# Performance work log

Hardware: AMD Instinct MI355X
Metric: run time of the kernel (lower is better)

The kernel has to match this reference:

```python
import jax, jax.numpy as jnp
import numpy as np

BS, NA, HW, C, HEADS = 16, 256, 1024, 512, 8
FEAT_RES = 32  # hw = feat_res**2


def setup_inputs() -> dict:
    key = jax.random.key(0)
    ks = jax.random.split(key, 16)

    def lin_w(k, din, dout):
        return (jax.random.normal(k, (din, dout), jnp.float32) / np.sqrt(din)).astype(jnp.float32)

    inp = {
        "tok_agent": jax.random.normal(ks[0], (BS, NA, C), jnp.float32),
        "enc_feat_supp": jax.random.normal(ks[1], (BS, HW, C), jnp.float32),
        "enc_feat_query": jax.random.normal(ks[2], (BS, HW, C), jnp.float32),
        # projection weights stored as [in, out]
        "W_qa": lin_w(ks[3], C, C), "b_qa": jnp.zeros((C,), jnp.float32),
        "W_ks": lin_w(ks[4], C, C), "b_ks": jnp.zeros((C,), jnp.float32),
        "W_ka": lin_w(ks[5], C, C), "b_ka": jnp.zeros((C,), jnp.float32),
        "W_vs": lin_w(ks[6], C, C), "b_vs": jnp.zeros((C,), jnp.float32),
        # FFN: c -> 3c -> c
        "W_f1": lin_w(ks[7], C, 3 * C), "b_f1": jnp.zeros((3 * C,), jnp.float32),
        "W_f2": lin_w(ks[8], 3 * C, C), "b_f2": jnp.zeros((C,), jnp.float32),
    }
    return inp


def reference(tok_agent, enc_feat_supp, enc_feat_query,
              W_qa, b_qa, W_ks, b_ks, W_ka, b_ka, W_vs, b_vs,
              W_f1, b_f1, W_f2, b_f2):
    bs, na, c = tok_agent.shape
    hw = enc_feat_supp.shape[1]
    feat_res = int(round(np.sqrt(hw)))
    d_k_sqrt = np.float32(np.sqrt(c // HEADS))

    qa = tok_agent @ W_qa + b_qa                 # [bs, na, c]
    ks_ = enc_feat_supp @ W_ks + b_ks            # [bs, hw, c]
    qq = enc_feat_query @ W_qa + b_qa            # NOTE: original reuses qa_linear
    ka = tok_agent @ W_ka + b_ka                 # [bs, na, c]
    vs = enc_feat_supp @ W_vs + b_vs             # [bs, hw, c]

    scores_as = jnp.einsum('bac,bhc->bah', qa, ks_) / d_k_sqrt   # [bs, na, hw]
    scores_qa = jnp.einsum('bhc,bac->bha', qq, ka) / d_k_sqrt    # [bs, hw, na]

    # align_mat[b,i,j] = (argmax_a scores_as[b,a,i] == argmax_a scores_qa[b,j,a])
    a_idx = jnp.argmax(scores_as, axis=1)        # [bs, hw]
    b_idx = jnp.argmax(scores_qa, axis=2)        # [bs, hw]
    align = jnp.where(a_idx[:, :, None] == b_idx[:, None, :],
                      jnp.float32(0.0), jnp.float32(-1e6))       # [bs, hw, hw]

    # scores_sa @ scores_aq: [bs,hw,na] @ [bs,na,hw]
    logits = jnp.einsum('bai,bja->bij', scores_as, scores_qa)    # [bs, hw, hw]
    scores_qs = jax.nn.softmax(logits + align, axis=-1)

    # scores_qs^T @ vs : out[b,j,c] = sum_i scores_qs[b,i,j] * vs[b,i,c]
    dec = jnp.einsum('bij,bic->bjc', scores_qs, vs)              # [bs, hw, c]
    dec = jax.nn.relu(dec @ W_f1 + b_f1) @ W_f2 + b_f2           # FFN (dropout = eval identity)

    # raw memory reinterpretation, as in torch .view
    return dec.reshape(bs, c, feat_res, -1)
```

## Files before the change

kernel.cpp:

```cpp
#include <hip/hip_runtime.h>

typedef float          f32x4  __attribute__((ext_vector_type(4)));
typedef short          bf16x8 __attribute__((ext_vector_type(8)));
typedef _Float16       f16x8  __attribute__((ext_vector_type(8)));
typedef unsigned short u16x4  __attribute__((ext_vector_type(4)));

static constexpr int kBS = 16;
static constexpr int kHW = 1024;

__device__ __forceinline__ unsigned short f2bf(float x) {
  union { float f; unsigned int u; } v; v.f = x;
  unsigned int r = v.u + 0x7fffu + ((v.u >> 16) & 1u);
  return (unsigned short)(r >> 16);
}
__device__ __forceinline__ float bf2f(unsigned short h) {
  union { unsigned int u; float f; } v; v.u = ((unsigned int)h) << 16;
  return v.f;
}
__device__ __forceinline__ unsigned short h2u(_Float16 h) {
  union { _Float16 h; unsigned short u; } v; v.h = h; return v.u;
}

__device__ __forceinline__ void split2h(float x, unsigned short& u0, unsigned short& u1) {
  _Float16 h0 = (_Float16)x;
  if (fabsf(x) < 6.1035156e-05f) h0 = (_Float16)0.f;
  const float r = (x - (float)h0) * 4096.f;
  u0 = h2u(h0);
  u1 = h2u((_Float16)r);
}

__global__ __launch_bounds__(256)
void split_act2h(const f32x4* __restrict__ X, u16x4* __restrict__ P0,
                 u16x4* __restrict__ P1, int n4)
{
  int i = blockIdx.x * 256 + threadIdx.x;
  if (i >= n4) return;
  f32x4 x = X[i];
  u16x4 s0, s1;
#pragma unroll
  for (int u = 0; u < 4; ++u) {
    unsigned short a, b;
    split2h(x[u], a, b);
    s0[u] = a; s1[u] = b;
  }
  P0[i] = s0; P1[i] = s1;
}

__global__ __launch_bounds__(256)
void split_wT2h(const float* __restrict__ Wm, unsigned short* __restrict__ T0,
                unsigned short* __restrict__ T1, int K, int N)
{
  __shared__ float ts[32][33];
  const int k0 = blockIdx.x * 32, n0 = blockIdx.y * 32;
  const int tx = threadIdx.x, ty = threadIdx.y;
#pragma unroll
  for (int r = 0; r < 4; ++r)
    ts[ty + r * 8][tx] = Wm[(size_t)(k0 + ty + r * 8) * N + n0 + tx];
  __syncthreads();
#pragma unroll
  for (int r = 0; r < 4; ++r) {
    const int n = ty + r * 8;
    const size_t off = (size_t)(n0 + n) * K + k0 + tx;
    unsigned short a, b;
    split2h(ts[tx][n], a, b);
    T0[off] = a; T1[off] = b;
  }
}

template<bool F16>
__global__ __launch_bounds__(256)
void split_wT1(const float* __restrict__ Wm, unsigned short* __restrict__ T0,
               int K, int N)
{
  __shared__ float ts[32][33];
  const int k0 = blockIdx.x * 32, n0 = blockIdx.y * 32;
  const int tx = threadIdx.x, ty = threadIdx.y;
#pragma unroll
  for (int r = 0; r < 4; ++r)
    ts[ty + r * 8][tx] = Wm[(size_t)(k0 + ty + r * 8) * N + n0 + tx];
  __syncthreads();
#pragma unroll
  for (int r = 0; r < 4; ++r) {
    const int n = ty + r * 8;
    const float x = ts[tx][n];
    const size_t off = (size_t)(n0 + n) * K + k0 + tx;
    T0[off] = F16 ? h2u((_Float16)x) : f2bf(x);
  }
}

__device__ __forceinline__ void stage_tile(const unsigned short* src, int K,
                                           unsigned short* ldst, int wv, int lane)
{
#pragma unroll
  for (int i = 0; i < 2; ++i) {
    const int s   = wv * 128 + i * 64 + lane;
    const int row = s >> 2;
    const int gc  = ((s & 3) ^ ((row >> 1) & 3)) * 8;
    __builtin_amdgcn_global_load_lds(
        (const __attribute__((address_space(1))) void*)(src + (size_t)row * K + gc),
        (__attribute__((address_space(3))) void*)(ldst + ((wv * 128 + i * 64) << 3)),
        16, 0, 0);
  }
}

template<int ORD, int KU, bool DBUF, int OUTM, bool BIAS, bool RELU, bool F16IN>
__global__ __launch_bounds__(256)
void gke(const unsigned short* __restrict__ A0, const unsigned short* __restrict__ A1,
         const unsigned short* __restrict__ B0, const unsigned short* __restrict__ B1,
         const float* __restrict__ bias,
         float* __restrict__ Cf, unsigned short* __restrict__ O0,
         unsigned short* __restrict__ O1,
         int K, int ldc, long sA, long sB, long sC, long sBias, float scale)
{
  constexpr int NP  = ORD + 1;
  constexpr int NT  = 2 * NP;
  constexpr int TPP = KU * NT;
  static_assert(!DBUF || TPP * 2 == 16, "vmcnt constant assumes 16 loads/phase");
  extern __shared__ __align__(16) unsigned short lds[];

  const int tid  = threadIdx.x;
  const int wv   = tid >> 6, lane = tid & 63;
  const int wr   = wv >> 1,  wc   = wv & 1;
  const int cr   = lane & 15, cg  = lane >> 4;
  const int bm   = blockIdx.x * 128, bn = blockIdx.y * 128;

  const size_t zA = (size_t)blockIdx.z * (size_t)sA;
  const size_t zB = (size_t)blockIdx.z * (size_t)sB;
  const size_t zC = (size_t)blockIdx.z * (size_t)sC;
  const size_t zBias = (size_t)blockIdx.z * (size_t)sBias;

  const unsigned short* srcs[NT];
  srcs[0] = A0 + zA + (size_t)bm * K;
  if (NP == 2) srcs[1] = A1 + zA + (size_t)bm * K;
  srcs[NP + 0] = B0 + zB + (size_t)bn * K;
  if (NP == 2) srcs[NP + 1] = B1 + zB + (size_t)bn * K;

  f32x4 acc0[4][4], acc1[4][4];
#pragma unroll
  for (int i = 0; i < 4; ++i)
#pragma unroll
    for (int j = 0; j < 4; ++j)
#pragma unroll
      for (int r = 0; r < 4; ++r) {
        acc0[i][j][r] = 0.f;
        if (ORD == 1) acc1[i][j][r] = 0.f;
      }

#define STAGE_PH(ph, buf)                                                       \
  {                                                                             \
    _Pragma("unroll")                                                           \
    for (int u = 0; u < KU; ++u)                                                \
      _Pragma("unroll")                                                         \
      for (int t = 0; t < NT; ++t)                                              \
        stage_tile(srcs[t] + ((ph) * KU + u) * 32, K,                           \
                   lds + (size_t)((buf) * TPP + u * NT + t) * 4096, wv, lane);  \
  }
#define LOADA(u, pa)                                                            \
  {                                                                             \
    _Pragma("unroll")                                                           \
    for (int f = 0; f < 4; ++f) {                                               \
      const int ra = wr * 64 + f * 16 + cr;                                     \
      af[f] = *(const bf16x8*)&lb[(size_t)((u) * NT + (pa)) * 4096 +            \
                                  (ra * 4 + (cg ^ ((ra >> 1) & 3))) * 8];       \
    }                                                                           \
  }
#define DOPB(u, pb, ACC)                                                        \
  {                                                                             \
    bf16x8 bfr[4];                                                              \
    _Pragma("unroll")                                                           \
    for (int f = 0; f < 4; ++f) {                                               \
      const int rb = wc * 64 + f * 16 + cr;                                     \
      bfr[f] = *(const bf16x8*)&lb[(size_t)((u) * NT + NP + (pb)) * 4096 +      \
                                   (rb * 4 + (cg ^ ((rb >> 1) & 3))) * 8];      \
    }                                                                           \
    _Pragma("unroll")                                                           \
    for (int i = 0; i < 4; ++i)                                                 \
      _Pragma("unroll")                                                         \
      for (int j = 0; j < 4; ++j) {                                             \
        if constexpr (F16IN)                                                    \
          ACC[i][j] = __builtin_amdgcn_mfma_f32_16x16x32_f16(                   \
              __builtin_bit_cast(f16x8, af[i]), __builtin_bit_cast(f16x8, bfr[j]), \
              ACC[i][j], 0, 0, 0);                                              \
        else                                                                    \
          ACC[i][j] = __builtin_amdgcn_mfma_f32_16x16x32_bf16(af[i], bfr[j],    \
              ACC[i][j], 0, 0, 0);                                              \
      }                                                                         \
  }
#define COMPUTE_PH(buf)                                                         \
  {                                                                             \
    const unsigned short* lb = lds + (size_t)(buf) * TPP * 4096;                \
    bf16x8 af[4];                                                               \
    _Pragma("unroll")                                                           \
    for (int u = 0; u < KU; ++u) {                                              \
      if constexpr (ORD == 1) {                                                 \
        LOADA(u, 0); DOPB(u, 0, acc0); DOPB(u, 1, acc1);                        \
        LOADA(u, 1); DOPB(u, 0, acc1);                                          \
      } else {                                                                  \
        LOADA(u, 0); DOPB(u, 0, acc0);                                          \
      }                                                                         \
    }                                                                           \
  }

  const int nph = K / (32 * KU);
  if constexpr (!DBUF) {
    for (int ph = 0; ph < nph; ++ph) {
      if (ph) __syncthreads();
      STAGE_PH(ph, 0);
      __syncthreads();
      COMPUTE_PH(0);
    }
  } else {
    STAGE_PH(0, 0);
    STAGE_PH(1, 1);
    for (int ph = 0; ph < nph; ++ph) {
      if (ph + 1 < nph) asm volatile("s_waitcnt vmcnt(16)" ::: "memory");
      else              asm volatile("s_waitcnt vmcnt(0)" ::: "memory");
      __builtin_amdgcn_sched_barrier(0);
      __builtin_amdgcn_s_barrier();
      COMPUTE_PH(ph & 1);
      __builtin_amdgcn_s_barrier();
      __builtin_amdgcn_sched_barrier(0);
      if (ph + 2 < nph) STAGE_PH(ph + 2, ph & 1);
    }
  }
#undef STAGE_PH
#undef LOADA
#undef DOPB
#undef COMPUTE_PH

  const float RS = 2.44140625e-4f;
  float* CfB = Cf + zC;
  unsigned short* O0B = O0 + zC;
  unsigned short* O1B = O1 + zC;
#pragma unroll
  for (int fm = 0; fm < 4; ++fm) {
#pragma unroll
    for (int fn = 0; fn < 4; ++fn) {
      const int n  = bn + wc * 64 + fn * 16 + cr;
      const int m0 = bm + wr * 64 + fm * 16 + 4 * cg;
      float bv = 0.f;
      if (BIAS) bv = bias[zBias + n];
      if (OUTM == 4) {
        u16x4 o;
#pragma unroll
        for (int r = 0; r < 4; ++r) {
          float x = acc0[fm][fn][r];
          if constexpr (ORD == 1) x += acc1[fm][fn][r] * RS;
          x = x * scale + bv;
          if (RELU) x = fmaxf(x, 0.f);
          o[r] = f2bf(x);
        }
        *(u16x4*)(O0B + (size_t)n * ldc + m0) = o;
      } else {
#pragma unroll
        for (int r = 0; r < 4; ++r) {
          float x = acc0[fm][fn][r];
          if constexpr (ORD == 1) x += acc1[fm][fn][r] * RS;
          x = x * scale + bv;
          if (RELU) x = fmaxf(x, 0.f);
          const size_t off = (size_t)(m0 + r) * ldc + n;
          if (OUTM == 0) CfB[off] = x;
          else if (OUTM == 3) O0B[off] = f2bf(x);
          else {
            unsigned short a, b;
            split2h(x, a, b);
            O0B[off] = a; O1B[off] = b;
            if (OUTM == 2) CfB[off] = x;
          }
        }
      }
    }
  }
}

__global__ __launch_bounds__(256)
void row_argmax4(const float* __restrict__ X, int* __restrict__ out)
{
  const int row = blockIdx.x * 4 + (threadIdx.x >> 6);
  const float* xr = X + (size_t)row * 256;
  const int lane = threadIdx.x & 63;
  float best = -3.0e38f;
  int bi = 0;
#pragma unroll
  for (int t = 0; t < 4; ++t) {
    const int a = lane + (t << 6);
    const float x = xr[a];
    if (x > best) { best = x; bi = a; }
  }
#pragma unroll
  for (int off = 32; off >= 1; off >>= 1) {
    const float ov = __shfl_xor(best, off);
    const int   oi = __shfl_xor(bi, off);
    if (ov > best || (ov == best && oi < bi)) { best = ov; bi = oi; }
  }
  if (lane == 0) out[row] = bi;
}

__global__ __launch_bounds__(256)
void softmax_T(const float* __restrict__ Lg, const int* __restrict__ aidx,
               const int* __restrict__ bidx, unsigned short* __restrict__ PT,
               int ihalf)
{
  __shared__ int bj[1024];
  __shared__ unsigned short tile[1024 * 17];
  const int tid = threadIdx.x;
  const int i0  = blockIdx.x * 16;
  const int b   = blockIdx.y;
  const int r   = tid >> 4;
  const int l16 = tid & 15;

  for (int j = tid; j < 1024; j += 256) bj[j] = bidx[(b << 10) + j];
  __syncthreads();

  const int ai  = aidx[(b << 10) + (ihalf << 9) + i0 + r];
  const float* Lr = Lg + ((size_t)b * 512 + i0 + r) * 1024;
  const int jb = l16 * 64;

  float x[64];
  float mx = -3.0e38f;
#pragma unroll
  for (int q = 0; q < 16; ++q) {
    f32x4 f = *(const f32x4*)(Lr + jb + (q << 2));
#pragma unroll
    for (int u = 0; u < 4; ++u) {
      const int j = jb + (q << 2) + u;
      float t = f[u];
      if (bj[j] != ai) t -= 1e6f;
      x[(q << 2) + u] = t;
      mx = fmaxf(mx, t);
    }
  }
#pragma unroll
  for (int off = 8; off >= 1; off >>= 1) mx = fmaxf(mx, __shfl_xor(mx, off));
  float s = 0.f;
#pragma unroll
  for (int k = 0; k < 64; ++k) { float e = expf(x[k] - mx); x[k] = e; s += e; }
#pragma unroll
  for (int off = 8; off >= 1; off >>= 1) s += __shfl_xor(s, off);
  const float inv = 1.f / s;

#pragma unroll
  for (int k = 0; k < 64; ++k)
    tile[(jb + k) * 17 + r] = f2bf(x[k] * inv);
  __syncthreads();

  for (int j = tid; j < 1024; j += 256) {
    const unsigned short* tp = &tile[j * 17];
    unsigned int w[8];
#pragma unroll
    for (int q = 0; q < 8; ++q)
      w[q] = (unsigned int)tp[2 * q] | ((unsigned int)tp[2 * q + 1] << 16);
    const size_t off = ((size_t)b << 20) + ((size_t)j << 10) + (ihalf << 9) + i0;
    unsigned int* dst = (unsigned int*)(PT + off);
    *(uint4*)dst       = make_uint4(w[0], w[1], w[2], w[3]);
    *((uint4*)dst + 1) = make_uint4(w[4], w[5], w[6], w[7]);
  }
}

extern "C" void kernel_launch(void* const* d_in, const int* in_sizes, int n_in,
                              void* d_out, int out_size, void* d_ws, size_t ws_size,
                              hipStream_t stream)
{
  (void)in_sizes; (void)n_in; (void)out_size; (void)ws_size;

  const float* tok  = (const float*)d_in[0];
  const float* supp = (const float*)d_in[1];
  const float* qry  = (const float*)d_in[2];
  const float* W_qa = (const float*)d_in[3];
  const float* b_qa = (const float*)d_in[4];
  const float* W_ks = (const float*)d_in[5];
  const float* b_ks = (const float*)d_in[6];
  const float* W_ka = (const float*)d_in[7];
  const float* b_ka = (const float*)d_in[8];
  const float* W_vs = (const float*)d_in[9];
  const float* b_vs = (const float*)d_in[10];
  const float* W_f1 = (const float*)d_in[11];
  const float* b_f1 = (const float*)d_in[12];
  const float* W_f2 = (const float*)d_in[13];
  const float* b_f2 = (const float*)d_in[14];

  auto kProj  = &gke<1,2,false,1,true ,false,true >;
  auto kScore = &gke<1,2,true ,2,false,false,true >;
  auto kLogit = &gke<1,2,false,0,false,false,true >;
  auto kVsT   = &gke<0,4,false,4,true ,false,true >;
  auto kPV    = &gke<0,4,false,3,false,false,false>;
  auto kFFN1  = &gke<0,4,false,3,true ,true ,false>;
  auto kFFN2  = &gke<0,4,false,0,true ,false,false>;
  hipFuncSetAttribute((const void*)kProj,  hipFuncAttributeMaxDynamicSharedMemorySize, 65536);
  hipFuncSetAttribute((const void*)kScore, hipFuncAttributeMaxDynamicSharedMemorySize, 131072);
  hipFuncSetAttribute((const void*)kLogit, hipFuncAttributeMaxDynamicSharedMemorySize, 65536);
  hipFuncSetAttribute((const void*)kVsT,   hipFuncAttributeMaxDynamicSharedMemorySize, 65536);
  hipFuncSetAttribute((const void*)kPV,    hipFuncAttributeMaxDynamicSharedMemorySize, 65536);
  hipFuncSetAttribute((const void*)kFFN1,  hipFuncAttributeMaxDynamicSharedMemorySize, 65536);
  hipFuncSetAttribute((const void*)kFFN2,  hipFuncAttributeMaxDynamicSharedMemorySize, 65536);

  char* W = (char*)d_ws;
  constexpr size_t MiB = 1048576;
  auto U = [&](double off) { return (unsigned short*)(W + (size_t)(off * MiB)); };
  auto F = [&](double off) { return (float*)(W + (size_t)(off * MiB)); };
  auto I = [&](double off) { return (int*)(W + (size_t)(off * MiB)); };

  const double oTOK0=0, oTOK1=4, oQTF=0, oSUP0=0, oSAF=0, oPT=0;
  const double oWQAT=16, oWKAT=17.5, oWKST=19, oWVST=20.5;
  const double oQA0=22, oQA1=26, oDEC=32, oKA0=34, oKA1=38;
  const double oQRY0=46, oQRY1=62, oQTP0=46, oQTP1=54;
  const double oSUP1=62, oVST=62, oSAP0=78, oSAP1=86;
  const double oQQ0=94, oQQ1=110, oLG=94, oMID=62;
  const double oWF1=142, oWF2=143.5, oBIA=148, oIDXB=150, oIDXA=150.0625;
  const double hP = 0.5;

  const dim3 B256(256), BW(32, 8);
  float* dummyF = F(oLG);
  unsigned short* dummyU = U(oLG);

  hipMemcpyAsync(W + (size_t)(oBIA * MiB), b_qa, 2048, hipMemcpyDeviceToDevice, stream);
  hipMemcpyAsync(W + (size_t)(oBIA * MiB) + 2048, b_ka, 2048, hipMemcpyDeviceToDevice, stream);

  split_wT2h<<<dim3(16,16), BW, 0, stream>>>(W_qa, U(oWQAT), U(oWQAT+hP), 512, 512);
  split_wT2h<<<dim3(16,16), BW, 0, stream>>>(W_ka, U(oWKAT), U(oWKAT+hP), 512, 512);
  split_wT2h<<<dim3(16,16), BW, 0, stream>>>(W_ks, U(oWKST), U(oWKST+hP), 512, 512);
  split_wT1<true><<<dim3(16,16), BW, 0, stream>>>(W_vs, U(oWVST), 512, 512);
  split_act2h<<<dim3(2048), B256, 0, stream>>>((const f32x4*)tok, (u16x4*)U(oTOK0), (u16x4*)U(oTOK1), 524288);
  kProj<<<dim3(32,4,2), B256, 65536, stream>>>(
      U(oTOK0),U(oTOK1), U(oWQAT),U(oWQAT+hP),
      F(oBIA), dummyF, U(oQA0),U(oQA1), 512, 512, 0, 786432, 6291456, 512, 1.f);
  split_act2h<<<dim3(8192), B256, 0, stream>>>((const f32x4*)qry, (u16x4*)U(oQRY0), (u16x4*)U(oQRY1), 2097152);
  kProj<<<dim3(128,4,1), B256, 65536, stream>>>(
      U(oQRY0),U(oQRY1), U(oWQAT),U(oWQAT+hP),
      b_qa, dummyF, U(oQQ0),U(oQQ1), 512, 512, 0,0,0,0, 1.f);
  kScore<<<dim3(8,2,16), B256, 131072, stream>>>(
      U(oQQ0),U(oQQ1), U(oKA0),U(oKA1),
      nullptr, F(oQTF), U(oQTP0),U(oQTP1), 512, 256,
      524288, 131072, 262144, 0, 0.125f);
  row_argmax4<<<dim3(kBS * kHW / 4), B256, 0, stream>>>(F(oQTF), I(oIDXB));
  split_act2h<<<dim3(8192), B256, 0, stream>>>((const f32x4*)supp, (u16x4*)U(oSUP0), (u16x4*)U(oSUP1), 2097152);
  kProj<<<dim3(128,4,1), B256, 65536, stream>>>(
      U(oSUP0),U(oSUP1), U(oWKST),U(oWKST+hP),
      b_ks, dummyF, U(oQQ0),U(oQQ1), 512, 512, 0,0,0,0, 1.f);
  kVsT<<<dim3(8,4,16), B256, 65536, stream>>>(
      U(oSUP0),dummyU, U(oWVST),dummyU,
      b_vs, dummyF, U(oVST),dummyU, 512, 1024,
      524288, 0, 524288, 0, 1.f);
  kScore<<<dim3(8,2,16), B256, 131072, stream>>>(
      U(oQQ0),U(oQQ1), U(oQA0),U(oQA1),
      nullptr, F(oSAF), U(oSAP0),U(oSAP1), 512, 256,
      524288, 131072, 262144, 0, 0.125f);
  row_argmax4<<<dim3(kBS * kHW / 4), B256, 0, stream>>>(F(oSAF), I(oIDXA));
  split_wT1<false><<<dim3(16,48), BW, 0, stream>>>(W_f1, U(oWF1), 512, 1536);
  split_wT1<false><<<dim3(48,16), BW, 0, stream>>>(W_f2, U(oWF2), 1536, 512);
  for (int h = 0; h < 2; ++h) {
    kLogit<<<dim3(4,8,16), B256, 65536, stream>>>(
        U(oSAP0) + (size_t)h*512*256, U(oSAP1) + (size_t)h*512*256,
        U(oQTP0), U(oQTP1),
        nullptr, F(oLG), dummyU,dummyU, 256, 1024,
        262144, 262144, 524288, 0, 1.f);
    softmax_T<<<dim3(32,16), B256, 0, stream>>>(F(oLG), I(oIDXA), I(oIDXB), U(oPT), h);
  }
  kPV<<<dim3(8,4,16), B256, 65536, stream>>>(
      U(oPT),dummyU, U(oVST),dummyU,
      nullptr, dummyF, U(oDEC),dummyU, 1024, 512,
      1048576, 524288, 524288, 0, 1.f);
  kFFN1<<<dim3(128,12,1), B256, 65536, stream>>>(
      U(oDEC),dummyU, U(oWF1),dummyU,
      b_f1, dummyF, U(oMID),dummyU, 512, 1536, 0,0,0,0, 1.f);
  kFFN2<<<dim3(128,4,1), B256, 65536, stream>>>(
      U(oMID),dummyU, U(oWF2),dummyU,
      b_f2, (float*)d_out, dummyU,dummyU, 1536, 512, 0,0,0,0, 1.f);
}
```

Baseline: 432.4 us.

## Generalize GEMM kernel to multi-stage async LDS pipeline for all launches

Replaces the boolean double-buffer flag with a DEPTH template parameter and a unified prefetch loop that keeps up to DEPTH k-phases in flight. Each wait uses a vmcnt literal matched to the loads per phase. Previously single-buffered GEMMs (projection, logits, PV, FFN) now use pipelined staging with smaller k-unroll per phase (2 or 4 stages), so global-load latency overlaps with MFMA work instead of being serialized by syncthreads. The LDS footprint per stage shrinks while the number of stages grows, so the existing shared-memory limits still fit. This adds more barriers per K iteration and relies on the hand-written vmcnt constants being correct.

```diff
diff --git a/kernel.cpp b/kernel.cpp
--- a/kernel.cpp
+++ b/kernel.cpp
@@ -103,7 +103,7 @@
   }
 }
 
-template<int ORD, int KU, bool DBUF, int OUTM, bool BIAS, bool RELU, bool F16IN>
+template<int ORD, int KU, int DEPTH, int OUTM, bool BIAS, bool RELU, bool F16IN>
 __global__ __launch_bounds__(256)
 void gke(const unsigned short* __restrict__ A0, const unsigned short* __restrict__ A1,
          const unsigned short* __restrict__ B0, const unsigned short* __restrict__ B1,
@@ -112,10 +112,12 @@
          unsigned short* __restrict__ O1,
          int K, int ldc, long sA, long sB, long sC, long sBias, float scale)
 {
-  constexpr int NP  = ORD + 1;
-  constexpr int NT  = 2 * NP;
-  constexpr int TPP = KU * NT;
-  static_assert(!DBUF || TPP * 2 == 16, "vmcnt constant assumes 16 loads/phase");
+  constexpr int NP   = ORD + 1;
+  constexpr int NT   = 2 * NP;
+  constexpr int TPP  = KU * NT;
+  constexpr int LPP  = TPP * 2;
+  static_assert(DEPTH == 2 || DEPTH == 4, "DEPTH in {2,4}");
+  static_assert(LPP == 4 || LPP == 8 || LPP == 16, "vmcnt literals");
   extern __shared__ __align__(16) unsigned short lds[];
 
   const int tid  = threadIdx.x;
@@ -202,26 +204,33 @@
   }
 
   const int nph = K / (32 * KU);
-  if constexpr (!DBUF) {
-    for (int ph = 0; ph < nph; ++ph) {
-      if (ph) __syncthreads();
-      STAGE_PH(ph, 0);
-      __syncthreads();
-      COMPUTE_PH(0);
+#pragma unroll
+  for (int d = 0; d < DEPTH; ++d)
+    if (d < nph) STAGE_PH(d, d);
+
+  for (int ph = 0; ph < nph; ++ph) {
+    const int rem = nph - 1 - ph;
+    const int fut = rem < (DEPTH - 1) ? rem : (DEPTH - 1);
+    if constexpr (LPP == 4) {
+      if (fut >= 3)      asm volatile("s_waitcnt vmcnt(12)" ::: "memory");
+      else if (fut == 2) asm volatile("s_waitcnt vmcnt(8)" ::: "memory");
+      else if (fut == 1) asm volatile("s_waitcnt vmcnt(4)" ::: "memory");
+      else               asm volatile("s_waitcnt vmcnt(0)" ::: "memory");
+    } else if constexpr (LPP == 8) {
+      if (fut >= 3)      asm volatile("s_waitcnt vmcnt(24)" ::: "memory");
+      else if (fut == 2) asm volatile("s_waitcnt vmcnt(16)" ::: "memory");
+      else if (fut == 1) asm volatile("s_waitcnt vmcnt(8)" ::: "memory");
+      else               asm volatile("s_waitcnt vmcnt(0)" ::: "memory");
+    } else {
+      if (fut >= 1)      asm volatile("s_waitcnt vmcnt(16)" ::: "memory");
+      else               asm volatile("s_waitcnt vmcnt(0)" ::: "memory");
     }
-  } else {
-    STAGE_PH(0, 0);
-    STAGE_PH(1, 1);
-    for (int ph = 0; ph < nph; ++ph) {
-      if (ph + 1 < nph) asm volatile("s_waitcnt vmcnt(16)" ::: "memory");
-      else              asm volatile("s_waitcnt vmcnt(0)" ::: "memory");
-      __builtin_amdgcn_sched_barrier(0);
-      __builtin_amdgcn_s_barrier();
-      COMPUTE_PH(ph & 1);
-      __builtin_amdgcn_s_barrier();
-      __builtin_amdgcn_sched_barrier(0);
-      if (ph + 2 < nph) STAGE_PH(ph + 2, ph & 1);
-    }
+    __builtin_amdgcn_sched_barrier(0);
+    __builtin_amdgcn_s_barrier();
+    COMPUTE_PH(ph & (DEPTH - 1));
+    __builtin_amdgcn_s_barrier();
+    __builtin_amdgcn_sched_barrier(0);
+    if (ph + DEPTH < nph) STAGE_PH(ph + DEPTH, ph & (DEPTH - 1));
   }
 #undef STAGE_PH
 #undef LOADA
@@ -379,13 +388,13 @@
   const float* W_f2 = (const float*)d_in[13];
   const float* b_f2 = (const float*)d_in[14];
 
-  auto kProj  = &gke<1,2,false,1,true ,false,true >;
-  auto kScore = &gke<1,2,true ,2,false,false,true >;
-  auto kLogit = &gke<1,2,false,0,false,false,true >;
-  auto kVsT   = &gke<0,4,false,4,true ,false,true >;
-  auto kPV    = &gke<0,4,false,3,false,false,false>;
-  auto kFFN1  = &gke<0,4,false,3,true ,true ,false>;
-  auto kFFN2  = &gke<0,4,false,0,true ,false,false>;
+  auto kProj  = &gke<1,1,2,1,true ,false,true >;
+  auto kScore = &gke<1,2,2,2,false,false,true >;
+  auto kLogit = &gke<1,1,2,0,false,false,true >;
+  auto kVsT   = &gke<0,1,4,4,true ,false,true >;
+  auto kPV    = &gke<0,1,4,3,false,false,false>;
+  auto kFFN1  = &gke<0,1,4,3,true ,true ,false>;
+  auto kFFN2  = &gke<0,1,4,0,true ,false,false>;
   hipFuncSetAttribute((const void*)kProj,  hipFuncAttributeMaxDynamicSharedMemorySize, 65536);
   hipFuncSetAttribute((const void*)kScore, hipFuncAttributeMaxDynamicSharedMemorySize, 131072);
   hipFuncSetAttribute((const void*)kLogit, hipFuncAttributeMaxDynamicSharedMemorySize, 65536);
```

Result: faster. 416.5 us (-3.7%).
